# Optimization experiments

Measured on AMD Instinct MI355X. Metric: run time of the kernel, lower is better.

## Reference

```python
import jax, jax.numpy as jnp
import numpy as np
from jax import lax

Q = 4          # decimation factor
N_ORDER = 8    # IIR filter order (scipy decimate default / explicit n=8)
RP = 0.05      # passband ripple in dB used by scipy.signal.decimate


def _cheby1_ba(N, rp, Wn):
    """Chebyshev type-I lowpass design, identical math to scipy.signal.cheby1."""
    eps = np.sqrt(10.0 ** (0.1 * rp) - 1.0)
    mu = np.arcsinh(1.0 / eps) / N
    k = np.arange(1, N + 1)
    theta = np.pi * (2 * k - 1) / (2 * N)
    # analog prototype poles (cheb1ap)
    p = -np.sinh(mu) * np.sin(theta) + 1j * np.cosh(mu) * np.cos(theta)
    g = np.prod(-p).real
    if N % 2 == 0:
        g /= np.sqrt(1.0 + eps ** 2)
    # frequency pre-warp (iirfilter with fs=2.0)
    fs = 2.0
    warped = 2.0 * fs * np.tan(np.pi * Wn / fs)
    # lp2lp_zpk
    p = p * warped
    g = g * warped ** N
    # bilinear_zpk
    fs2 = 2.0 * fs
    pd = (fs2 + p) / (fs2 - p)
    zd = -np.ones(N)  # N zeros at z=-1
    gd = g * np.real(1.0 / np.prod(fs2 - p))
    b = np.real(gd * np.poly(zd))
    a = np.real(np.poly(pd))
    return b, a


def _lfilter_zi(b, a):
    """Steady-state initial conditions, identical math to scipy.signal.lfilter_zi."""
    n = len(a)
    comp = np.zeros((n - 1, n - 1))
    comp[0, :] = -a[1:] / a[0]
    comp[1:, :-1] = np.eye(n - 2)
    IminusA = np.eye(n - 1) - comp.T
    B = b[1:] - a[1:] * b[0]
    return np.linalg.solve(IminusA, B)


_B_NP, _A_NP = _cheby1_ba(N_ORDER, RP, 0.8 / Q)
_ZI_NP = _lfilter_zi(_B_NP, _A_NP)


def _lfilter(b, a, x, zi):
    """IIR filter, direct-form II transposed. x: (T, M), zi: (order, M)."""
    def step(z, xt):
        yt = b[0] * xt + z[0]                       # (M,)
        z = jnp.concatenate([z[1:], jnp.zeros_like(z[:1])], axis=0) \
            + b[1:, None] * xt[None, :] - a[1:, None] * yt[None, :]
        return z, yt
    _, y = lax.scan(step, zi, x)
    return y


def _filtfilt(b, a, zi, x):
    """scipy.signal.filtfilt with padtype='odd', padlen=3*max(len(a),len(b)). x: (T, M)."""
    edge = 3 * b.shape[0]  # 27 for an order-8 filter
    left = 2.0 * x[0] - x[edge:0:-1]            # odd extension, left
    right = 2.0 * x[-1] - x[-2:-(edge + 2):-1]  # odd extension, right
    ext = jnp.concatenate([left, x, right], axis=0)
    y = _lfilter(b, a, ext, zi[:, None] * ext[0][None, :])          # forward pass
    y = _lfilter(b, a, y[::-1], zi[:, None] * y[-1][None, :])[::-1]  # backward pass
    return y[edge:-edge]


def _decimate(x):
    """scipy.signal.decimate(x, q=Q, n=8, ftype='iir', axis=-1, zero_phase=True)."""
    B_, C_, T = x.shape
    b = jnp.asarray(_B_NP, x.dtype)
    a = jnp.asarray(_A_NP, x.dtype)
    zi = jnp.asarray(_ZI_NP, x.dtype)
    xt = x.reshape(B_ * C_, T).T  # (T, M) -- time leading for lax.scan
    y = _filtfilt(b, a, zi, xt)
    y = y.T.reshape(B_, C_, T)
    return y[..., ::Q]


def setup_inputs() -> dict:
    key = jax.random.key(0)
    x = jax.random.normal(key, (32, 16, 65536), dtype=jnp.float32)
    return {"x": x}


def reference(x):
    return _decimate(x)
```

## Files before the change

kernel.cpp:

```cpp
#include <hip/hip_runtime.h>
#include <cmath>
#include <complex>

namespace {

constexpr int TLEN   = 65536;
constexpr int NCH    = 512;
constexpr int LEXT   = TLEN + 54;
constexpr int NCHUNK = 257;
constexpr int PAD    = 5;
constexpr int ROWS4  = 16416;
constexpr size_t BUF_FLOATS = (size_t)ROWS4 * 2048;


struct Coefs {
  float b0,b1,b2,b3,b4,b5,b6,b7,b8;
  float na1,na2,na3,na4,na5,na6,na7,na8;
  float zi0,zi1,zi2,zi3,zi4,zi5,zi6,zi7;
};

#define IIR_STEP(xv, yv)                                  \
  do {                                                    \
    yv = fmaf(cf.b0, (xv), z0);                           \
    z0 = fmaf(cf.na1, yv, fmaf(cf.b1, (xv), z1));         \
    z1 = fmaf(cf.na2, yv, fmaf(cf.b2, (xv), z2));         \
    z2 = fmaf(cf.na3, yv, fmaf(cf.b3, (xv), z3));         \
    z3 = fmaf(cf.na4, yv, fmaf(cf.b4, (xv), z4));         \
    z4 = fmaf(cf.na5, yv, fmaf(cf.b5, (xv), z5));         \
    z5 = fmaf(cf.na6, yv, fmaf(cf.b6, (xv), z6));         \
    z6 = fmaf(cf.na7, yv, fmaf(cf.b7, (xv), z7));         \
    z7 = fmaf(cf.na8, yv, cf.b8 * (xv));                  \
  } while (0)

__global__ __launch_bounds__(256) void k_transpose(const float* __restrict__ x,
                                                   float* __restrict__ ext) {
  __shared__ float lds[64 * 260];
  const int bx = blockIdx.x;
  const int m0 = blockIdx.y * 64;
  const int tid = threadIdx.x;
  const int t0 = bx * 256;
#pragma unroll
  for (int i = 0; i < 16; ++i) {
    int idx = tid + i * 256;
    int ch = idx >> 6;
    int tq = idx & 63;
    float4 v = *reinterpret_cast<const float4*>(
        x + (size_t)(m0 + ch) * TLEN + t0 + tq * 4);
    *reinterpret_cast<float4*>(&lds[ch * 260 + tq * 4]) = v;
  }
  __syncthreads();
#pragma unroll
  for (int i = 0; i < 16; ++i) {
    int idx = tid + i * 256;
    int j = idx >> 6;
    int ch = idx & 63;
    float4 v = *reinterpret_cast<const float4*>(&lds[ch * 260 + j * 4]);
    *reinterpret_cast<float4*>(
        ext + (size_t)(64 * bx + 8 + j) * 2048 + (size_t)(m0 + ch) * 4) = v;
  }
}

__global__ void k_edges(const float* __restrict__ x, float* __restrict__ ext) {
  const int r = blockIdx.x;
  const int m = threadIdx.x;
  int e, src;
  float base;
  if (r < 27) {
    e = r; src = 27 - r;
    base = x[(size_t)m * TLEN];
  } else {
    int j = r - 27;
    e = TLEN + 27 + j; src = TLEN - 2 - j;
    base = x[(size_t)m * TLEN + (TLEN - 1)];
  }
  float v = 2.0f * base - x[(size_t)m * TLEN + src];
  int s = e + PAD;
  ext[(size_t)(s >> 2) * 2048 + (size_t)m * 4 + (s & 3)] = v;
}

__global__ __launch_bounds__(256) void k_fwd(const float* __restrict__ ext,
                                             float* __restrict__ yb, Coefs cf) {
  const int m = blockIdx.y * 256 + threadIdx.x;
  const int c = blockIdx.x;
  float z0, z1, z2, z3, z4, z5, z6, z7;
  int s4_begin, store_s4;
  if (c == 0) {
    float x0 = ext[(size_t)1 * 2048 + (size_t)m * 4 + 1];
    z0 = cf.zi0 * x0; z1 = cf.zi1 * x0; z2 = cf.zi2 * x0; z3 = cf.zi3 * x0;
    z4 = cf.zi4 * x0; z5 = cf.zi5 * x0; z6 = cf.zi6 * x0; z7 = cf.zi7 * x0;
#pragma unroll
    for (int s = 5; s < 8; ++s) {
      float xin = ext[(size_t)(s >> 2) * 2048 + (size_t)m * 4 + (s & 3)];
      float yv; IIR_STEP(xin, yv);
      yb[(size_t)(s >> 2) * 2048 + (size_t)m * 4 + (s & 3)] = yv;
    }
    s4_begin = 2; store_s4 = 2;
  } else {
    s4_begin = 64 * c - 62;
    float x0 = ext[(size_t)s4_begin * 2048 + (size_t)m * 4];
    z0 = cf.zi0 * x0; z1 = cf.zi1 * x0; z2 = cf.zi2 * x0; z3 = cf.zi3 * x0;
    z4 = cf.zi4 * x0; z5 = cf.zi5 * x0; z6 = cf.zi6 * x0; z7 = cf.zi7 * x0;
    store_s4 = 64 * c + 1;
  }
  const int s4_last = min(64 * c + 64, 16398);
  const float4* xv = reinterpret_cast<const float4*>(ext);
  float4* yv = reinterpret_cast<float4*>(yb);
  float4 b0 = xv[(size_t)(s4_begin + 0) * 512 + m];
  float4 b1 = xv[(size_t)(s4_begin + 1) * 512 + m];
  float4 b2 = xv[(size_t)(s4_begin + 2) * 512 + m];
  float4 b3 = xv[(size_t)(s4_begin + 3) * 512 + m];
  float4 b4 = xv[(size_t)(s4_begin + 4) * 512 + m];
  float4 b5 = xv[(size_t)(s4_begin + 5) * 512 + m];
  float4 b6 = xv[(size_t)(s4_begin + 6) * 512 + m];
  float4 b7 = xv[(size_t)(s4_begin + 7) * 512 + m];
  for (int g = s4_begin; g <= s4_last; g += 4) {
    float4 c0 = b0, c1 = b1, c2 = b2, c3 = b3;
    b0 = b4; b1 = b5; b2 = b6; b3 = b7;
    b4 = xv[(size_t)(g + 8) * 512 + m];
    b5 = xv[(size_t)(g + 9) * 512 + m];
    b6 = xv[(size_t)(g + 10) * 512 + m];
    b7 = xv[(size_t)(g + 11) * 512 + m];
#pragma unroll
    for (int j = 0; j < 4; ++j) {
      float4 xq = (j == 0) ? c0 : (j == 1) ? c1 : (j == 2) ? c2 : c3;
      const int sg = g + j;
      float4 o;
      IIR_STEP(xq.x, o.x);
      IIR_STEP(xq.y, o.y);
      IIR_STEP(xq.z, o.z);
      IIR_STEP(xq.w, o.w);
      if (sg >= store_s4 && sg <= s4_last)
        yv[(size_t)sg * 512 + m] = o;
    }
  }
}

__global__ __launch_bounds__(256) void k_bwd(const float* __restrict__ yb,
                                             float* __restrict__ ot2, Coefs cf) {
  const int m = blockIdx.y * 256 + threadIdx.x;
  const int c = blockIdx.x;
  const int own_lo = 256 * c;
  float z0, z1, z2, z3, z4, z5, z6, z7;
  int g_begin;
  if (c <= 1) {
    float y0 = yb[(size_t)16398 * 2048 + (size_t)m * 4 + 2];
    z0 = cf.zi0 * y0; z1 = cf.zi1 * y0; z2 = cf.zi2 * y0; z3 = cf.zi3 * y0;
    z4 = cf.zi4 * y0; z5 = cf.zi5 * y0; z6 = cf.zi6 * y0; z7 = cf.zi7 * y0;
#pragma unroll
    for (int s = 65594; s >= 65584; --s) {
      float yin = yb[(size_t)(s >> 2) * 2048 + (size_t)m * 4 + (s & 3)];
      float wv; IIR_STEP(yin, wv);
      (void)wv;
    }
    g_begin = 16395;
  } else {
    g_begin = 16463 - 64 * c;
    float y0 = yb[(size_t)g_begin * 2048 + (size_t)m * 4 + 3];
    z0 = cf.zi0 * y0; z1 = cf.zi1 * y0; z2 = cf.zi2 * y0; z3 = cf.zi3 * y0;
    z4 = cf.zi4 * y0; z5 = cf.zi5 * y0; z6 = cf.zi6 * y0; z7 = cf.zi7 * y0;
  }
  const int g_stop = max(1, 16334 - 64 * c);
  const float4* yv = reinterpret_cast<const float4*>(yb);
  auto ld = [&](int r) {
    int rr = r < 0 ? 0 : r;
    return yv[(size_t)rr * 512 + m];
  };
  float4 b0 = ld(g_begin), b1 = ld(g_begin - 1), b2 = ld(g_begin - 2), b3 = ld(g_begin - 3);
  float4 b4 = ld(g_begin - 4), b5 = ld(g_begin - 5), b6 = ld(g_begin - 6), b7 = ld(g_begin - 7);
  for (int g = g_begin; g >= g_stop; g -= 4) {
    float4 c0 = b0, c1 = b1, c2 = b2, c3 = b3;
    b0 = b4; b1 = b5; b2 = b6; b3 = b7;
    b4 = ld(g - 8); b5 = ld(g - 9); b6 = ld(g - 10); b7 = ld(g - 11);
    float4 pack;
#pragma unroll
    for (int j = 0; j < 4; ++j) {
      float4 q = (j == 0) ? c0 : (j == 1) ? c1 : (j == 2) ? c2 : c3;
      float w3, w2, w1, w0;
      IIR_STEP(q.w, w3);
      IIR_STEP(q.z, w2);
      IIR_STEP(q.y, w1);
      IIR_STEP(q.x, w0);
      (void)w3; (void)w2; (void)w1;
      if (j == 0) pack.w = w0;
      else if (j == 1) pack.z = w0;
      else if (j == 2) pack.y = w0;
      else pack.x = w0;
    }
    if (65594 - 4 * g >= own_lo && g >= 11 && g <= 16391)
      *reinterpret_cast<float4*>(ot2 + (size_t)((g - 11) >> 2) * 2048 + (size_t)m * 4) = pack;
  }
}

__global__ __launch_bounds__(256) void k_outT(const float* __restrict__ ot2,
                                              float* __restrict__ out) {
  __shared__ float4 lds4[64 * 65];
  const int q0 = blockIdx.x * 64;
  const int m0 = blockIdx.y * 64;
  const int tid = threadIdx.x;
#pragma unroll
  for (int i = 0; i < 16; ++i) {
    int idx = tid + i * 256;
    int ql = idx >> 6;
    int ml = idx & 63;
    lds4[ql * 65 + ml] = *reinterpret_cast<const float4*>(
        ot2 + (size_t)(q0 + ql) * 2048 + (size_t)(m0 + ml) * 4);
  }
  __syncthreads();
#pragma unroll
  for (int i = 0; i < 16; ++i) {
    int idx = tid + i * 256;
    int ml = idx >> 6;
    int ql = idx & 63;
    float4 v = lds4[ql * 65 + ml];
    *reinterpret_cast<float4*>(
        out + (size_t)(m0 + ml) * 16384 + (size_t)(q0 + ql) * 4) = v;
  }
}

static void solve8(double Mm[8][9], double* zi) {
  for (int col = 0; col < 8; ++col) {
    int piv = col;
    for (int r = col + 1; r < 8; ++r)
      if (std::fabs(Mm[r][col]) > std::fabs(Mm[piv][col])) piv = r;
    if (piv != col)
      for (int j = 0; j < 9; ++j) { double t = Mm[col][j]; Mm[col][j] = Mm[piv][j]; Mm[piv][j] = t; }
    double d = Mm[col][col];
    for (int j = col; j < 9; ++j) Mm[col][j] /= d;
    for (int r = 0; r < 8; ++r)
      if (r != col) {
        double f = Mm[r][col];
        if (f != 0.0)
          for (int j = col; j < 9; ++j) Mm[r][j] -= f * Mm[col][j];
      }
  }
  for (int i = 0; i < 8; ++i) zi[i] = Mm[i][8];
}

static Coefs make_coefs() {
  using cd = std::complex<double>;
  const int N = 8;
  const double rp = 0.05, Wn = 0.8 / 4.0;
  double eps = std::sqrt(std::pow(10.0, 0.1 * rp) - 1.0);
  double mu = std::asinh(1.0 / eps) / N;
  cd p[8];
  for (int i = 0; i < N; ++i) {
    double th = M_PI * (2.0 * (i + 1) - 1.0) / (2.0 * N);
    p[i] = cd(-std::sinh(mu) * std::sin(th), std::cosh(mu) * std::cos(th));
  }
  cd pr(1.0, 0.0);
  for (int i = 0; i < N; ++i) pr *= -p[i];
  double g = pr.real();
  g /= std::sqrt(1.0 + eps * eps);
  const double fs = 2.0;
  double warped = 2.0 * fs * std::tan(M_PI * Wn / fs);
  for (int i = 0; i < N; ++i) p[i] *= warped;
  g *= std::pow(warped, (double)N);
  const double fs2 = 2.0 * fs;
  cd pd[8], dpr(1.0, 0.0);
  for (int i = 0; i < N; ++i) {
    pd[i] = (cd(fs2, 0.0) + p[i]) / (cd(fs2, 0.0) - p[i]);
    dpr *= (cd(fs2, 0.0) - p[i]);
  }
  double gd = g * (cd(1.0, 0.0) / dpr).real();
  static const double binom[9] = {1, 8, 28, 56, 70, 56, 28, 8, 1};
  double b[9], a[9];
  for (int i = 0; i < 9; ++i) b[i] = gd * binom[i];
  cd cp[9]; cp[0] = cd(1, 0);
  for (int i = 1; i < 9; ++i) cp[i] = cd(0, 0);
  for (int i = 0; i < N; ++i)
    for (int j = i + 1; j >= 1; --j) cp[j] -= pd[i] * cp[j - 1];
  for (int i = 0; i < 9; ++i) a[i] = cp[i].real();
  double Mm[8][9];
  for (int i = 0; i < 8; ++i) {
    for (int j = 0; j < 9; ++j) Mm[i][j] = 0.0;
    Mm[i][0] += a[i + 1];
    Mm[i][i] += 1.0;
    if (i < 7) Mm[i][i + 1] = -1.0;
    Mm[i][8] = b[i + 1] - a[i + 1] * b[0];
  }
  double zi[8];
  solve8(Mm, zi);
  Coefs cf;
  cf.b0 = (float)b[0]; cf.b1 = (float)b[1]; cf.b2 = (float)b[2]; cf.b3 = (float)b[3];
  cf.b4 = (float)b[4]; cf.b5 = (float)b[5]; cf.b6 = (float)b[6]; cf.b7 = (float)b[7];
  cf.b8 = (float)b[8];
  cf.na1 = (float)(-a[1]); cf.na2 = (float)(-a[2]); cf.na3 = (float)(-a[3]);
  cf.na4 = (float)(-a[4]); cf.na5 = (float)(-a[5]); cf.na6 = (float)(-a[6]);
  cf.na7 = (float)(-a[7]); cf.na8 = (float)(-a[8]);
  cf.zi0 = (float)zi[0]; cf.zi1 = (float)zi[1]; cf.zi2 = (float)zi[2]; cf.zi3 = (float)zi[3];
  cf.zi4 = (float)zi[4]; cf.zi5 = (float)zi[5]; cf.zi6 = (float)zi[6]; cf.zi7 = (float)zi[7];
  return cf;
}

}

extern "C" void kernel_launch(void* const* d_in, const int* in_sizes, int n_in,
                              void* d_out, int out_size, void* d_ws, size_t ws_size,
                              hipStream_t stream) {
  (void)in_sizes; (void)n_in; (void)out_size; (void)ws_size;
  const float* x = (const float*)d_in[0];
  float* out = (float*)d_out;
  float* ext = (float*)d_ws;
  float* yb  = ext + BUF_FLOATS;
  float* ot2 = ext;
  Coefs cf = make_coefs();
  hipLaunchKernelGGL(k_transpose, dim3(TLEN / 256, NCH / 64), dim3(256), 0, stream, x, ext);
  hipLaunchKernelGGL(k_edges, dim3(54), dim3(512), 0, stream, x, ext);
  hipLaunchKernelGGL(k_fwd, dim3(NCHUNK, 2), dim3(256), 0, stream, ext, yb, cf);
  hipLaunchKernelGGL(k_bwd, dim3(NCHUNK, 2), dim3(256), 0, stream, yb, ot2, cf);
  hipLaunchKernelGGL(k_outT, dim3(4096 / 64, NCH / 64), dim3(256), 0, stream, ot2, out);
}
```

Baseline: 335.2 us.

## Fuse transpose and edge padding into forward IIR pass with LDS staging

Removes the separate transpose and odd-extension edge kernels. The forward filter now reads the original channel-major input directly, transposes it through a triple-buffered LDS tile, and computes edge samples on the fly. Chunks become longer (512 samples with a warm-up overlap) and each block handles 64 channels. Only one wavefront of each block does the recurrence while the other threads prefetch, which cuts parallelism during the serial IIR and risks lower occupancy and throughput. This saves a full write and read of the extended buffer.

```diff
diff --git a/kernel.cpp b/kernel.cpp
--- a/kernel.cpp
+++ b/kernel.cpp
@@ -7,10 +7,8 @@
 constexpr int TLEN   = 65536;
 constexpr int NCH    = 512;
 constexpr int LEXT   = TLEN + 54;
-constexpr int NCHUNK = 257;
 constexpr int PAD    = 5;
-constexpr int ROWS4  = 16416;
-constexpr size_t BUF_FLOATS = (size_t)ROWS4 * 2048;
+constexpr size_t YB_ROWS = 16400;
 
 
 struct Coefs {
@@ -32,107 +30,118 @@
     z7 = fmaf(cf.na8, yv, cf.b8 * (xv));                  \
   } while (0)
 
-__global__ __launch_bounds__(256) void k_transpose(const float* __restrict__ x,
-                                                   float* __restrict__ ext) {
-  __shared__ float lds[64 * 260];
-  const int bx = blockIdx.x;
+template<int QOFF, bool VEC>
+__device__ __forceinline__ void run_chunk(const float* __restrict__ x,
+                                          float* __restrict__ yb,
+                                          const Coefs& cf,
+                                          float (&lds)[3][4160],
+                                          int m0, int e0, int nsub,
+                                          int store_lo, int store_hi) {
+  const int tid  = threadIdx.x;
+  const int lane = tid & 63;
+  const int vtbase = e0 - 27;
+  const int mIdx = m0 + lane;
+  float4* yq = reinterpret_cast<float4*>(yb);
+  const int tq  = tid & 15;
+  const int chb = tid >> 4;
+  float4 rr0, rr1, rr2, rr3;
+  float rs[16];
+
+  auto issue = [&](int k) {
+    const int vt0 = vtbase + 64 * k;
+    if (VEC) {
+      const float* p = x + (size_t)(m0 + chb) * TLEN + vt0 + 4 * tq;
+      rr0 = *reinterpret_cast<const float4*>(p);
+      rr1 = *reinterpret_cast<const float4*>(p + (size_t)16 * TLEN);
+      rr2 = *reinterpret_cast<const float4*>(p + (size_t)32 * TLEN);
+      rr3 = *reinterpret_cast<const float4*>(p + (size_t)48 * TLEN);
+    } else {
+#pragma unroll
+      for (int i = 0; i < 16; ++i) {
+        int idx = tid + 256 * i;
+        int tl = idx & 63, ch = idx >> 6;
+        int vt = vt0 + tl;
+        const float* xr = x + (size_t)(m0 + ch) * TLEN;
+        float v;
+        if (vt < 0) v = 2.0f * xr[0] - xr[-vt];
+        else if (vt >= TLEN) v = 2.0f * xr[TLEN - 1] - xr[2 * TLEN - 2 - vt];
+        else v = xr[vt];
+        rs[i] = v;
+      }
+    }
+  };
+  auto commit = [&](int k) {
+    float* b = lds[k % 3];
+    if (VEC) {
+      const int base = 4 * tq * 65;
+      b[base       + chb     ] = rr0.x; b[base + 65  + chb     ] = rr0.y;
+      b[base + 130 + chb     ] = rr0.z; b[base + 195 + chb     ] = rr0.w;
+      b[base       + chb + 16] = rr1.x; b[base + 65  + chb + 16] = rr1.y;
+      b[base + 130 + chb + 16] = rr1.z; b[base + 195 + chb + 16] = rr1.w;
+      b[base       + chb + 32] = rr2.x; b[base + 65  + chb + 32] = rr2.y;
+      b[base + 130 + chb + 32] = rr2.z; b[base + 195 + chb + 32] = rr2.w;
+      b[base       + chb + 48] = rr3.x; b[base + 65  + chb + 48] = rr3.y;
+      b[base + 130 + chb + 48] = rr3.z; b[base + 195 + chb + 48] = rr3.w;
+    } else {
+#pragma unroll
+      for (int i = 0; i < 16; ++i) {
+        int idx = tid + 256 * i;
+        int tl = idx & 63, ch = idx >> 6;
+        b[tl * 65 + ch] = rs[i];
+      }
+    }
+  };
+
+  issue(0); commit(0);
+  issue(1); commit(1);
+
+  float z0 = 0, z1 = 0, z2 = 0, z3 = 0, z4 = 0, z5 = 0, z6 = 0, z7 = 0;
+  float4 oq = make_float4(0.f, 0.f, 0.f, 0.f);
+
+  for (int k = 0; k < nsub; ++k) {
+    __syncthreads();
+    if (k == 0 && tid < 64) {
+      float x0 = lds[0][lane];
+      z0 = cf.zi0 * x0; z1 = cf.zi1 * x0; z2 = cf.zi2 * x0; z3 = cf.zi3 * x0;
+      z4 = cf.zi4 * x0; z5 = cf.zi5 * x0; z6 = cf.zi6 * x0; z7 = cf.zi7 * x0;
+    }
+    if (k + 2 < nsub) issue(k + 2);
+    if (tid < 64) {
+      const float* tile = lds[k % 3];
+#pragma unroll
+      for (int tl = 0; tl < 64; ++tl) {
+        float xin = tile[tl * 65 + lane];
+        float yv; IIR_STEP(xin, yv);
+        if (QOFF == 1) {
+          if (k == 0 && tl < 3) yb[2048 + mIdx * 4 + tl + 1] = yv;
+        }
+        const int q = (tl + QOFF) & 3;
+        if (q == 0) oq.x = yv;
+        else if (q == 1) oq.y = yv;
+        else if (q == 2) oq.z = yv;
+        else {
+          oq.w = yv;
+          const int step = 64 * k + tl;
+          if (step >= store_lo && step <= store_hi)
+            yq[(size_t)((e0 + step + 5) >> 2) * 512 + mIdx] = oq;
+        }
+      }
+    }
+    if (k + 2 < nsub) commit(k + 2);
+  }
+}
+
+__global__ __launch_bounds__(256) void k_fwd2(const float* __restrict__ x,
+                                              float* __restrict__ yb, Coefs cf) {
+  __shared__ float lds[3][4160];
+  const int c  = blockIdx.x;
   const int m0 = blockIdx.y * 64;
-  const int tid = threadIdx.x;
-  const int t0 = bx * 256;
-#pragma unroll
-  for (int i = 0; i < 16; ++i) {
-    int idx = tid + i * 256;
-    int ch = idx >> 6;
-    int tq = idx & 63;
-    float4 v = *reinterpret_cast<const float4*>(
-        x + (size_t)(m0 + ch) * TLEN + t0 + tq * 4);
-    *reinterpret_cast<float4*>(&lds[ch * 260 + tq * 4]) = v;
-  }
-  __syncthreads();
-#pragma unroll
-  for (int i = 0; i < 16; ++i) {
-    int idx = tid + i * 256;
-    int j = idx >> 6;
-    int ch = idx & 63;
-    float4 v = *reinterpret_cast<const float4*>(&lds[ch * 260 + j * 4]);
-    *reinterpret_cast<float4*>(
-        ext + (size_t)(64 * bx + 8 + j) * 2048 + (size_t)(m0 + ch) * 4) = v;
-  }
-}
-
-__global__ void k_edges(const float* __restrict__ x, float* __restrict__ ext) {
-  const int r = blockIdx.x;
-  const int m = threadIdx.x;
-  int e, src;
-  float base;
-  if (r < 27) {
-    e = r; src = 27 - r;
-    base = x[(size_t)m * TLEN];
-  } else {
-    int j = r - 27;
-    e = TLEN + 27 + j; src = TLEN - 2 - j;
-    base = x[(size_t)m * TLEN + (TLEN - 1)];
-  }
-  float v = 2.0f * base - x[(size_t)m * TLEN + src];
-  int s = e + PAD;
-  ext[(size_t)(s >> 2) * 2048 + (size_t)m * 4 + (s & 3)] = v;
-}
-
-__global__ __launch_bounds__(256) void k_fwd(const float* __restrict__ ext,
-                                             float* __restrict__ yb, Coefs cf) {
-  const int m = blockIdx.y * 256 + threadIdx.x;
-  const int c = blockIdx.x;
-  float z0, z1, z2, z3, z4, z5, z6, z7;
-  int s4_begin, store_s4;
-  if (c == 0) {
-    float x0 = ext[(size_t)1 * 2048 + (size_t)m * 4 + 1];
-    z0 = cf.zi0 * x0; z1 = cf.zi1 * x0; z2 = cf.zi2 * x0; z3 = cf.zi3 * x0;
-    z4 = cf.zi4 * x0; z5 = cf.zi5 * x0; z6 = cf.zi6 * x0; z7 = cf.zi7 * x0;
-#pragma unroll
-    for (int s = 5; s < 8; ++s) {
-      float xin = ext[(size_t)(s >> 2) * 2048 + (size_t)m * 4 + (s & 3)];
-      float yv; IIR_STEP(xin, yv);
-      yb[(size_t)(s >> 2) * 2048 + (size_t)m * 4 + (s & 3)] = yv;
-    }
-    s4_begin = 2; store_s4 = 2;
-  } else {
-    s4_begin = 64 * c - 62;
-    float x0 = ext[(size_t)s4_begin * 2048 + (size_t)m * 4];
-    z0 = cf.zi0 * x0; z1 = cf.zi1 * x0; z2 = cf.zi2 * x0; z3 = cf.zi3 * x0;
-    z4 = cf.zi4 * x0; z5 = cf.zi5 * x0; z6 = cf.zi6 * x0; z7 = cf.zi7 * x0;
-    store_s4 = 64 * c + 1;
-  }
-  const int s4_last = min(64 * c + 64, 16398);
-  const float4* xv = reinterpret_cast<const float4*>(ext);
-  float4* yv = reinterpret_cast<float4*>(yb);
-  float4 b0 = xv[(size_t)(s4_begin + 0) * 512 + m];
-  float4 b1 = xv[(size_t)(s4_begin + 1) * 512 + m];
-  float4 b2 = xv[(size_t)(s4_begin + 2) * 512 + m];
-  float4 b3 = xv[(size_t)(s4_begin + 3) * 512 + m];
-  float4 b4 = xv[(size_t)(s4_begin + 4) * 512 + m];
-  float4 b5 = xv[(size_t)(s4_begin + 5) * 512 + m];
-  float4 b6 = xv[(size_t)(s4_begin + 6) * 512 + m];
-  float4 b7 = xv[(size_t)(s4_begin + 7) * 512 + m];
-  for (int g = s4_begin; g <= s4_last; g += 4) {
-    float4 c0 = b0, c1 = b1, c2 = b2, c3 = b3;
-    b0 = b4; b1 = b5; b2 = b6; b3 = b7;
-    b4 = xv[(size_t)(g + 8) * 512 + m];
-    b5 = xv[(size_t)(g + 9) * 512 + m];
-    b6 = xv[(size_t)(g + 10) * 512 + m];
-    b7 = xv[(size_t)(g + 11) * 512 + m];
-#pragma unroll
-    for (int j = 0; j < 4; ++j) {
-      float4 xq = (j == 0) ? c0 : (j == 1) ? c1 : (j == 2) ? c2 : c3;
-      const int sg = g + j;
-      float4 o;
-      IIR_STEP(xq.x, o.x);
-      IIR_STEP(xq.y, o.y);
-      IIR_STEP(xq.z, o.z);
-      IIR_STEP(xq.w, o.w);
-      if (sg >= store_s4 && sg <= s4_last)
-        yv[(size_t)sg * 512 + m] = o;
-    }
-  }
+  if (c == 0)
+    run_chunk<1, false>(x, yb, cf, lds, m0, 0, 8, 6, 510);
+  else if (c == 128)
+    run_chunk<0, false>(x, yb, cf, lds, m0, 65283, 5, 255, 307);
+  else
+    run_chunk<0, true>(x, yb, cf, lds, m0, 512 * c - 253, 12, 255, 763);
 }
 
 __global__ __launch_bounds__(256) void k_bwd(const float* __restrict__ yb,
@@ -300,13 +309,10 @@
   (void)in_sizes; (void)n_in; (void)out_size; (void)ws_size;
   const float* x = (const float*)d_in[0];
   float* out = (float*)d_out;
-  float* ext = (float*)d_ws;
-  float* yb  = ext + BUF_FLOATS;
-  float* ot2 = ext;
+  float* yb  = (float*)d_ws;
+  float* ot2 = yb + YB_ROWS * 2048;
   Coefs cf = make_coefs();
-  hipLaunchKernelGGL(k_transpose, dim3(TLEN / 256, NCH / 64), dim3(256), 0, stream, x, ext);
-  hipLaunchKernelGGL(k_edges, dim3(54), dim3(512), 0, stream, x, ext);
-  hipLaunchKernelGGL(k_fwd, dim3(NCHUNK, 2), dim3(256), 0, stream, ext, yb, cf);
-  hipLaunchKernelGGL(k_bwd, dim3(NCHUNK, 2), dim3(256), 0, stream, yb, ot2, cf);
+  hipLaunchKernelGGL(k_fwd2, dim3(129, NCH / 64), dim3(256), 0, stream, x, yb, cf);
+  hipLaunchKernelGGL(k_bwd, dim3(257, 2), dim3(256), 0, stream, yb, ot2, cf);
   hipLaunchKernelGGL(k_outT, dim3(4096 / 64, NCH / 64), dim3(256), 0, stream, ot2, out);
 }
```

After: 311.5 us. 1.08x faster.
